# Kernel tuning notes

Hardware: AMD Instinct MI355X
Metric: run time of the kernel (lower is better)

The kernel has to match this reference:

```python
import jax, jax.numpy as jnp
import numpy as np

B, S, H, E = 32, 2048, 1024, 1024
NEG = -10000000000.0


def setup_inputs() -> dict:
    key = jax.random.key(0)
    ks = jax.random.split(key, 8)
    scale = 1.0 / np.sqrt(H)
    return {
        "hidden": jax.random.normal(ks[0], (B, H), jnp.float32),
        "encoder_outputs": jax.random.normal(ks[1], (B, S, E), jnp.float32),
        "mask": jax.random.randint(ks[2], (B, S), 0, 2, jnp.int32),
        "W_h": jax.random.normal(ks[3], (H, H), jnp.float32) * scale,
        "b_h": jax.random.normal(ks[4], (H,), jnp.float32) * scale,
        "W_e": jax.random.normal(ks[5], (E, H), jnp.float32) * scale,
        "b_e": jax.random.normal(ks[6], (H,), jnp.float32) * scale,
        "v": jax.random.normal(ks[7], (H,), jnp.float32) * scale,
    }


def reference(hidden, encoder_outputs, mask, W_h, b_h, W_e, b_e, v):
    # hidden proj: (B,H) -> (B,1,H); encoder proj: (B,S,E) -> (B,S,H)
    h_proj = (hidden @ W_h + b_h)[:, None, :]
    e_proj = jnp.einsum("bse,eh->bsh", encoder_outputs, W_e) + b_e
    energy = jnp.tanh(h_proj + e_proj)                      # (B,S,H)
    attention = jnp.einsum("bsh,h->bs", energy, v)          # (B,S)
    attention = jnp.where(mask == 0, NEG, attention)
    attention_weights = jax.nn.softmax(attention, axis=1)   # (B,S)
    context = jnp.einsum("bs,bse->be", attention_weights, encoder_outputs)
    return (context, attention_weights)
```

## Files before the change

kernel.cpp:

```cpp
#include <hip/hip_runtime.h>

#define NEGV -10000000000.0f

typedef _Float16 half8 __attribute__((ext_vector_type(8)));
typedef float f32x4 __attribute__((ext_vector_type(4)));

__device__ __forceinline__ void gld16(const void* g, void* l) {
  __builtin_amdgcn_global_load_lds((const __attribute__((address_space(1))) void*)g,
                                   (__attribute__((address_space(3))) void*)l,
                                   16, 0, 0);
}

__device__ __forceinline__ float fast_tanh(float x) {
  const float e = __expf(2.0f * x);
  return 1.0f - 2.0f * __builtin_amdgcn_rcpf(e + 1.0f);
}

__global__ __launch_bounds__(256) void prep_kernel(
    const float* __restrict__ enc, _Float16* __restrict__ enc16,
    const float* __restrict__ We, _Float16* __restrict__ W16T,
    const float* __restrict__ hidden, const float* __restrict__ W_h,
    const float* __restrict__ b_h, const float* __restrict__ b_e,
    float* __restrict__ hpb) {
  __shared__ float tile[32][33];
  const int bid = blockIdx.x;
  const int tid = threadIdx.x;

  if (bid < 128) {
    const int b = bid >> 2;
    const int h = ((bid & 3) << 8) | tid;
    const float* hb = hidden + b * 1024;
    float a0 = 0.f, a1 = 0.f, a2 = 0.f, a3 = 0.f;
    #pragma unroll 4
    for (int k = 0; k < 1024; k += 4) {
      a0 = fmaf(hb[k + 0], W_h[(size_t)(k + 0) * 1024 + h], a0);
      a1 = fmaf(hb[k + 1], W_h[(size_t)(k + 1) * 1024 + h], a1);
      a2 = fmaf(hb[k + 2], W_h[(size_t)(k + 2) * 1024 + h], a2);
      a3 = fmaf(hb[k + 3], W_h[(size_t)(k + 3) * 1024 + h], a3);
    }
    hpb[b * 1024 + h] = b_h[h] + b_e[h] + ((a0 + a1) + (a2 + a3));
  } else if (bid < 128 + 1024) {
    const int tb = bid - 128;
    const int n0 = (tb & 31) << 5, k0 = (tb >> 5) << 5;
    const int tx = tid & 31, ty = tid >> 5;
    #pragma unroll
    for (int i = 0; i < 4; ++i) {
      const int r = ty + (i << 3);
      tile[r][tx] = We[(size_t)(k0 + r) * 1024 + n0 + tx];
    }
    __syncthreads();
    #pragma unroll
    for (int i = 0; i < 4; ++i) {
      const int r = ty + (i << 3);
      W16T[(size_t)(n0 + r) * 1024 + k0 + tx] = (_Float16)tile[tx][r];
    }
  } else {
    const size_t base = ((size_t)(bid - 1152) * 256 + tid) * 8;
    const float4 x = *(const float4*)(enc + base);
    const float4 y = *(const float4*)(enc + base + 4);
    half8 h;
    h[0] = (_Float16)x.x; h[1] = (_Float16)x.y; h[2] = (_Float16)x.z; h[3] = (_Float16)x.w;
    h[4] = (_Float16)y.x; h[5] = (_Float16)y.y; h[6] = (_Float16)y.z; h[7] = (_Float16)y.w;
    *(half8*)(enc16 + base) = h;
  }
}

__global__ __launch_bounds__(512, 2) void attn_gemm8_kernel(
    const _Float16* __restrict__ enc16, const _Float16* __restrict__ W16T,
    const float* __restrict__ hpb, const float* __restrict__ v,
    const int* __restrict__ mask, float* __restrict__ logits) {
  __shared__ __align__(16) _Float16 Abuf[2][2][256 * 32];
  __shared__ __align__(16) _Float16 Bbuf[2][2][256 * 32];
  __shared__ float hp_s[1024];
  __shared__ float vh_s[1024];
  __shared__ float red[1024];

  const int tid = threadIdx.x;
  const int wid = tid >> 6;
  const int lane = tid & 63;
  const int l15 = lane & 15;
  const int qq = lane >> 4;
  const int wr = wid >> 2;
  const int wc = wid & 3;
  const int m0 = blockIdx.x << 8;
  const int b = blockIdx.x >> 3;

  for (int i = tid; i < 1024; i += 512) {
    hp_s[i] = hpb[(b << 10) + i];
    vh_s[i] = v[i];
  }

  const int r0 = tid >> 2;
  const int r1 = r0 + 128;
  const int g0 = tid & 3;
  const int sc = (g0 ^ ((r0 >> 1) & 3)) << 4;
  const int ldsoff0 = (wid << 10);
  const int ldsoff1 = (wid << 10) + 8192;

  const char* encb = (const char*)(enc16 + (size_t)m0 * 1024);
  const char* wb0 = (const char*)W16T;

  auto stageA = [&](int par, int kh, int t) {
    const int colb = ((t & 15) << 7) + (kh << 6) + sc;
    char* base = (char*)(&Abuf[par][kh][0]);
    gld16(encb + (size_t)r0 * 2048 + colb, base + ldsoff0);
    gld16(encb + (size_t)r1 * 2048 + colb, base + ldsoff1);
  };
  auto stageB = [&](int par, int kh, int t) {
    const char* wb = wb0 + ((size_t)(t >> 4) << 19);
    const int colb = ((t & 15) << 7) + (kh << 6) + sc;
    char* base = (char*)(&Bbuf[par][kh][0]);
    gld16(wb + (size_t)r0 * 2048 + colb, base + ldsoff0);
    gld16(wb + (size_t)r1 * 2048 + colb, base + ldsoff1);
  };

  int aoff[2][4], boff[4];
  #pragma unroll
  for (int mh = 0; mh < 2; ++mh)
    #pragma unroll
    for (int mi = 0; mi < 4; ++mi) {
      const int row = (wr << 7) + (mh << 6) + (mi << 4) + l15;
      aoff[mh][mi] = (row << 6) + ((qq ^ ((row >> 1) & 3)) << 4);
    }
  #pragma unroll
  for (int ni = 0; ni < 4; ++ni) {
    const int np = (wc << 6) + (ni << 4) + l15;
    boff[ni] = (np << 6) + ((qq ^ ((np >> 1) & 3)) << 4);
  }

  f32x4 acc[8][4];
  float rowsum[8][4];
  #pragma unroll
  for (int mi = 0; mi < 8; ++mi)
    #pragma unroll
    for (int j = 0; j < 4; ++j) {
      acc[mi][j] = (f32x4){0.f, 0.f, 0.f, 0.f};
      rowsum[mi][j] = 0.f;
    }

  stageA(0, 0, 0); stageB(0, 0, 0);
  stageA(0, 1, 0); stageB(0, 1, 0);
  asm volatile("s_waitcnt vmcnt(4)" ::: "memory");
  __builtin_amdgcn_s_barrier();

  #pragma unroll 1
  for (int t = 0; t < 64; ++t) {
    const int par = t & 1, npar = par ^ 1;
    const bool more = t < 63;
    half8 a[4], bf[4];

    {
      const char* A0 = (const char*)(&Abuf[par][0][0]);
      const char* B0 = (const char*)(&Bbuf[par][0][0]);
      #pragma unroll
      for (int mi = 0; mi < 4; ++mi) a[mi] = *(const half8*)(A0 + aoff[0][mi]);
      #pragma unroll
      for (int ni = 0; ni < 4; ++ni) bf[ni] = *(const half8*)(B0 + boff[ni]);
      if (more) { stageA(npar, 0, t + 1); stageB(npar, 0, t + 1); }
      __builtin_amdgcn_s_setprio(1);
      #pragma unroll
      for (int mi = 0; mi < 4; ++mi)
        #pragma unroll
        for (int ni = 0; ni < 4; ++ni)
          acc[mi][ni] = __builtin_amdgcn_mfma_f32_16x16x32_f16(a[mi], bf[ni], acc[mi][ni], 0, 0, 0);
      __builtin_amdgcn_s_setprio(0);
      #pragma unroll
      for (int mi = 0; mi < 4; ++mi) a[mi] = *(const half8*)(A0 + aoff[1][mi]);
      __builtin_amdgcn_s_setprio(1);
      #pragma unroll
      for (int mi = 0; mi < 4; ++mi)
        #pragma unroll
        for (int ni = 0; ni < 4; ++ni)
          acc[4 + mi][ni] = __builtin_amdgcn_mfma_f32_16x16x32_f16(a[mi], bf[ni], acc[4 + mi][ni], 0, 0, 0);
      __builtin_amdgcn_s_setprio(0);
      if (more) asm volatile("s_waitcnt vmcnt(4)" ::: "memory");
      else      asm volatile("s_waitcnt vmcnt(0)" ::: "memory");
      __builtin_amdgcn_s_barrier();
    }

    {
      const char* A1 = (const char*)(&Abuf[par][1][0]);
      const char* B1 = (const char*)(&Bbuf[par][1][0]);
      #pragma unroll
      for (int mi = 0; mi < 4; ++mi) a[mi] = *(const half8*)(A1 + aoff[0][mi]);
      #pragma unroll
      for (int ni = 0; ni < 4; ++ni) bf[ni] = *(const half8*)(B1 + boff[ni]);
      if (more) { stageA(npar, 1, t + 1); stageB(npar, 1, t + 1); }
      __builtin_amdgcn_s_setprio(1);
      #pragma unroll
      for (int mi = 0; mi < 4; ++mi)
        #pragma unroll
        for (int ni = 0; ni < 4; ++ni)
          acc[mi][ni] = __builtin_amdgcn_mfma_f32_16x16x32_f16(a[mi], bf[ni], acc[mi][ni], 0, 0, 0);
      __builtin_amdgcn_s_setprio(0);
      #pragma unroll
      for (int mi = 0; mi < 4; ++mi) a[mi] = *(const half8*)(A1 + aoff[1][mi]);
      __builtin_amdgcn_s_setprio(1);
      #pragma unroll
      for (int mi = 0; mi < 4; ++mi)
        #pragma unroll
        for (int ni = 0; ni < 4; ++ni)
          acc[4 + mi][ni] = __builtin_amdgcn_mfma_f32_16x16x32_f16(a[mi], bf[ni], acc[4 + mi][ni], 0, 0, 0);
      __builtin_amdgcn_s_setprio(0);
      if (more) asm volatile("s_waitcnt vmcnt(4)" ::: "memory");
      __builtin_amdgcn_s_barrier();
    }

    if ((t & 15) == 15) {
      const int nt = t >> 4;
      const int hb = (nt << 8) + (wc << 6);
      #pragma unroll
      for (int ni = 0; ni < 4; ++ni) {
        const int h = hb + (ni << 4) + l15;
        const float hv = hp_s[h];
        const float vv = vh_s[h];
        #pragma unroll
        for (int mi = 0; mi < 8; ++mi) {
          #pragma unroll
          for (int r = 0; r < 4; ++r)
            rowsum[mi][r] += fast_tanh(acc[mi][ni][r] + hv) * vv;
          acc[mi][ni] = (f32x4){0.f, 0.f, 0.f, 0.f};
        }
      }
    }
  }

  #pragma unroll
  for (int mi = 0; mi < 8; ++mi)
    #pragma unroll
    for (int r = 0; r < 4; ++r) {
      float s = rowsum[mi][r];
      s += __shfl_xor(s, 1);
      s += __shfl_xor(s, 2);
      s += __shfl_xor(s, 4);
      s += __shfl_xor(s, 8);
      rowsum[mi][r] = s;
    }
  __syncthreads();
  if (l15 == 0) {
    #pragma unroll
    for (int mi = 0; mi < 8; ++mi)
      #pragma unroll
      for (int r = 0; r < 4; ++r) {
        const int row = (wr << 7) + (mi << 4) + (qq << 2) + r;
        red[(row << 2) + wc] = rowsum[mi][r];
      }
  }
  __syncthreads();
  if (tid < 256) {
    const float s = red[tid << 2] + red[(tid << 2) + 1] + red[(tid << 2) + 2] + red[(tid << 2) + 3];
    const int m = m0 + tid;
    logits[m] = (mask[(b << 11) + (m & 2047)] == 0) ? NEGV : s;
  }
}

__global__ void softmax_kernel(const float* __restrict__ logits, float* __restrict__ wout) {
  __shared__ float red[4];
  const int b = blockIdx.x, tid = threadIdx.x;
  const int wid = tid >> 6, lane = tid & 63;
  const float* lb = logits + b * 2048;
  float x[8];
  #pragma unroll
  for (int j = 0; j < 8; ++j) x[j] = lb[tid + j * 256];
  float m = x[0];
  #pragma unroll
  for (int j = 1; j < 8; ++j) m = fmaxf(m, x[j]);
  #pragma unroll
  for (int off = 32; off > 0; off >>= 1) m = fmaxf(m, __shfl_xor(m, off));
  if (lane == 0) red[wid] = m;
  __syncthreads();
  m = fmaxf(fmaxf(red[0], red[1]), fmaxf(red[2], red[3]));
  __syncthreads();
  float e[8];
  float s = 0.f;
  #pragma unroll
  for (int j = 0; j < 8; ++j) { e[j] = expf(x[j] - m); s += e[j]; }
  #pragma unroll
  for (int off = 32; off > 0; off >>= 1) s += __shfl_xor(s, off);
  if (lane == 0) red[wid] = s;
  __syncthreads();
  s = red[0] + red[1] + red[2] + red[3];
  const float inv = 1.0f / s;
  #pragma unroll
  for (int j = 0; j < 8; ++j) wout[b * 2048 + tid + j * 256] = e[j] * inv;
}

__global__ void context16_kernel(const _Float16* __restrict__ enc16,
                                 const float* __restrict__ wout, float* __restrict__ ctx) {
  const int b = blockIdx.x >> 4;
  const int ch = blockIdx.x & 15;
  const int tl = threadIdx.x & 127;
  const int sh = threadIdx.x >> 7;
  float a[8] = {0.f, 0.f, 0.f, 0.f, 0.f, 0.f, 0.f, 0.f};
  #pragma unroll 1
  for (int i = 0; i < 64; ++i) {
    const int s = (ch << 7) + (i << 1) + sh;
    const float w = wout[(b << 11) + s];
    const half8 r = *(const half8*)(enc16 + (((size_t)(b << 11) + s) << 10) + (tl << 3));
    #pragma unroll
    for (int j = 0; j < 8; ++j) a[j] = fmaf(w, (float)r[j], a[j]);
  }
  float* c = ctx + (b << 10) + (tl << 3);
  #pragma unroll
  for (int j = 0; j < 8; ++j) atomicAdd(c + j, a[j]);
}

extern "C" void kernel_launch(void* const* d_in, const int* in_sizes, int n_in,
                              void* d_out, int out_size, void* d_ws, size_t ws_size,
                              hipStream_t stream) {
  const float* hidden = (const float*)d_in[0];
  const float* enc    = (const float*)d_in[1];
  const int*   mask   = (const int*)d_in[2];
  const float* W_h    = (const float*)d_in[3];
  const float* b_h    = (const float*)d_in[4];
  const float* W_e    = (const float*)d_in[5];
  const float* b_e    = (const float*)d_in[6];
  const float* v      = (const float*)d_in[7];

  float* ctx  = (float*)d_out;
  float* wout = (float*)d_out + 32 * 1024;

  char* ws = (char*)d_ws;
  const size_t ENC16_BYTES = 134217728ULL;
  _Float16* enc16 = (_Float16*)ws;
  _Float16* W16T  = (_Float16*)(ws + ENC16_BYTES);
  float* hpb      = (float*)(ws + ENC16_BYTES + 2097152);
  float* logits   = (float*)(ws + ENC16_BYTES + 2097152 + 131072);

  hipMemsetAsync(ctx, 0, 32 * 1024 * sizeof(float), stream);
  hipLaunchKernelGGL(prep_kernel, dim3(1152 + 32768), dim3(256), 0, stream,
                     enc, enc16, W_e, W16T, hidden, W_h, b_h, b_e, hpb);
  hipLaunchKernelGGL(attn_gemm8_kernel, dim3(256), dim3(512), 0, stream,
                     enc16, W16T, hpb, v, mask, logits);
  hipLaunchKernelGGL(softmax_kernel, dim3(32), dim3(256), 0, stream, logits, wout);
  hipLaunchKernelGGL(context16_kernel, dim3(512), dim3(256), 0, stream, enc16, wout, ctx);
}
```

Measured before the change: 318.6 us.

## Restructure GEMM K-loop into triple-buffered 32-wide stages with split A/B prefetch

Replaces the double-buffered loop over 64-wide K steps, each split into two halves, with a triple-buffered ring of 32-wide K tiles. Loads run two stages ahead. The A and B prefetches are issued separately, each placed between two barriers around the MFMA blocks. The aim is to hide global-to-LDS latency better and to interleave loads with compute, at the cost of more barriers per unit of K.

```diff
diff --git a/kernel.cpp b/kernel.cpp
--- a/kernel.cpp
+++ b/kernel.cpp
@@ -69,8 +69,8 @@
     const _Float16* __restrict__ enc16, const _Float16* __restrict__ W16T,
     const float* __restrict__ hpb, const float* __restrict__ v,
     const int* __restrict__ mask, float* __restrict__ logits) {
-  __shared__ __align__(16) _Float16 Abuf[2][2][256 * 32];
-  __shared__ __align__(16) _Float16 Bbuf[2][2][256 * 32];
+  __shared__ __align__(16) _Float16 Abuf[3][256 * 32];
+  __shared__ __align__(16) _Float16 Bbuf[3][256 * 32];
   __shared__ float hp_s[1024];
   __shared__ float vh_s[1024];
   __shared__ float red[1024];
@@ -100,16 +100,16 @@
   const char* encb = (const char*)(enc16 + (size_t)m0 * 1024);
   const char* wb0 = (const char*)W16T;
 
-  auto stageA = [&](int par, int kh, int t) {
-    const int colb = ((t & 15) << 7) + (kh << 6) + sc;
-    char* base = (char*)(&Abuf[par][kh][0]);
+  auto stageA = [&](int buf, int t) {
+    const int colb = ((t & 31) << 6) + sc;
+    char* base = (char*)(&Abuf[buf][0]);
     gld16(encb + (size_t)r0 * 2048 + colb, base + ldsoff0);
     gld16(encb + (size_t)r1 * 2048 + colb, base + ldsoff1);
   };
-  auto stageB = [&](int par, int kh, int t) {
-    const char* wb = wb0 + ((size_t)(t >> 4) << 19);
-    const int colb = ((t & 15) << 7) + (kh << 6) + sc;
-    char* base = (char*)(&Bbuf[par][kh][0]);
+  auto stageB = [&](int buf, int t) {
+    const char* wb = wb0 + ((size_t)(t >> 5) << 19);
+    const int colb = ((t & 31) << 6) + sc;
+    char* base = (char*)(&Bbuf[buf][0]);
     gld16(wb + (size_t)r0 * 2048 + colb, base + ldsoff0);
     gld16(wb + (size_t)r1 * 2048 + colb, base + ldsoff1);
   };
@@ -138,76 +138,53 @@
       rowsum[mi][j] = 0.f;
     }
 
-  stageA(0, 0, 0); stageB(0, 0, 0);
-  stageA(0, 1, 0); stageB(0, 1, 0);
-  asm volatile("s_waitcnt vmcnt(4)" ::: "memory");
-  __builtin_amdgcn_s_barrier();
-
+  stageA(0, 0); stageB(0, 0);
+  stageA(1, 1); stageB(1, 1);
+  __syncthreads();
+
+  int bi = 0;
   #pragma unroll 1
-  for (int t = 0; t < 64; ++t) {
-    const int par = t & 1, npar = par ^ 1;
-    const bool more = t < 63;
+  for (int t = 0; t < 128; ++t) {
+    const int bi2 = (bi >= 1) ? bi - 1 : bi + 2;
+    const char* A = (const char*)(&Abuf[bi][0]);
+    const char* B = (const char*)(&Bbuf[bi][0]);
     half8 a[4], bf[4];
 
-    {
-      const char* A0 = (const char*)(&Abuf[par][0][0]);
-      const char* B0 = (const char*)(&Bbuf[par][0][0]);
+    #pragma unroll
+    for (int mi = 0; mi < 4; ++mi) a[mi] = *(const half8*)(A + aoff[0][mi]);
+    #pragma unroll
+    for (int ni = 0; ni < 4; ++ni) bf[ni] = *(const half8*)(B + boff[ni]);
+    if (t < 126) stageA(bi2, t + 2);
+    __builtin_amdgcn_s_barrier();
+    asm volatile("s_waitcnt lgkmcnt(0)" ::: "memory");
+    __builtin_amdgcn_s_setprio(1);
+    #pragma unroll
+    for (int mi = 0; mi < 4; ++mi)
       #pragma unroll
-      for (int mi = 0; mi < 4; ++mi) a[mi] = *(const half8*)(A0 + aoff[0][mi]);
+      for (int ni = 0; ni < 4; ++ni)
+        acc[mi][ni] = __builtin_amdgcn_mfma_f32_16x16x32_f16(a[mi], bf[ni], acc[mi][ni], 0, 0, 0);
+    __builtin_amdgcn_s_setprio(0);
+    __builtin_amdgcn_s_barrier();
+
+    #pragma unroll
+    for (int mi = 0; mi < 4; ++mi) a[mi] = *(const half8*)(A + aoff[1][mi]);
+    if (t < 126) stageB(bi2, t + 2);
+    __builtin_amdgcn_s_barrier();
+    asm volatile("s_waitcnt lgkmcnt(0)" ::: "memory");
+    __builtin_amdgcn_s_setprio(1);
+    #pragma unroll
+    for (int mi = 0; mi < 4; ++mi)
       #pragma unroll
-      for (int ni = 0; ni < 4; ++ni) bf[ni] = *(const half8*)(B0 + boff[ni]);
-      if (more) { stageA(npar, 0, t + 1); stageB(npar, 0, t + 1); }
-      __builtin_amdgcn_s_setprio(1);
-      #pragma unroll
-      for (int mi = 0; mi < 4; ++mi)
-        #pragma unroll
-        for (int ni = 0; ni < 4; ++ni)
-          acc[mi][ni] = __builtin_amdgcn_mfma_f32_16x16x32_f16(a[mi], bf[ni], acc[mi][ni], 0, 0, 0);
-      __builtin_amdgcn_s_setprio(0);
-      #pragma unroll
-      for (int mi = 0; mi < 4; ++mi) a[mi] = *(const half8*)(A0 + aoff[1][mi]);
-      __builtin_amdgcn_s_setprio(1);
-      #pragma unroll
-      for (int mi = 0; mi < 4; ++mi)
-        #pragma unroll
-        for (int ni = 0; ni < 4; ++ni)
-          acc[4 + mi][ni] = __builtin_amdgcn_mfma_f32_16x16x32_f16(a[mi], bf[ni], acc[4 + mi][ni], 0, 0, 0);
-      __builtin_amdgcn_s_setprio(0);
-      if (more) asm volatile("s_waitcnt vmcnt(4)" ::: "memory");
-      else      asm volatile("s_waitcnt vmcnt(0)" ::: "memory");
-      __builtin_amdgcn_s_barrier();
-    }
-
-    {
-      const char* A1 = (const char*)(&Abuf[par][1][0]);
-      const char* B1 = (const char*)(&Bbuf[par][1][0]);
-      #pragma unroll
-      for (int mi = 0; mi < 4; ++mi) a[mi] = *(const half8*)(A1 + aoff[0][mi]);
-      #pragma unroll
-      for (int ni = 0; ni < 4; ++ni) bf[ni] = *(const half8*)(B1 + boff[ni]);
-      if (more) { stageA(npar, 1, t + 1); stageB(npar, 1, t + 1); }
-      __builtin_amdgcn_s_setprio(1);
-      #pragma unroll
-      for (int mi = 0; mi < 4; ++mi)
-        #pragma unroll
-        for (int ni = 0; ni < 4; ++ni)
-          acc[mi][ni] = __builtin_amdgcn_mfma_f32_16x16x32_f16(a[mi], bf[ni], acc[mi][ni], 0, 0, 0);
-      __builtin_amdgcn_s_setprio(0);
-      #pragma unroll
-      for (int mi = 0; mi < 4; ++mi) a[mi] = *(const half8*)(A1 + aoff[1][mi]);
-      __builtin_amdgcn_s_setprio(1);
-      #pragma unroll
-      for (int mi = 0; mi < 4; ++mi)
-        #pragma unroll
-        for (int ni = 0; ni < 4; ++ni)
-          acc[4 + mi][ni] = __builtin_amdgcn_mfma_f32_16x16x32_f16(a[mi], bf[ni], acc[4 + mi][ni], 0, 0, 0);
-      __builtin_amdgcn_s_setprio(0);
-      if (more) asm volatile("s_waitcnt vmcnt(4)" ::: "memory");
-      __builtin_amdgcn_s_barrier();
-    }
-
-    if ((t & 15) == 15) {
-      const int nt = t >> 4;
+      for (int ni = 0; ni < 4; ++ni)
+        acc[4 + mi][ni] = __builtin_amdgcn_mfma_f32_16x16x32_f16(a[mi], bf[ni], acc[4 + mi][ni], 0, 0, 0);
+    __builtin_amdgcn_s_setprio(0);
+
+    if (t < 126) asm volatile("s_waitcnt vmcnt(4)" ::: "memory");
+    else         asm volatile("s_waitcnt vmcnt(0)" ::: "memory");
+    __builtin_amdgcn_s_barrier();
+
+    if ((t & 31) == 31) {
+      const int nt = t >> 5;
       const int hb = (nt << 8) + (wc << 6);
       #pragma unroll
       for (int ni = 0; ni < 4; ++ni) {
@@ -223,6 +200,7 @@
         }
       }
     }
+    bi = (bi >= 2) ? 0 : bi + 1;
   }
 
   #pragma unroll
```

New measurement: 292.1 us, median of 3. 1.09x faster.
